# Optimization experiments

Hardware: AMD Instinct MI355X
Metric: run time of the kernel (lower is better)

## Reference

```python
import jax, jax.numpy as jnp
import numpy as np

B, D, H = 32768, 256, 256
LEAKY = 0.2  # tf.nn.leaky_relu default alpha


def setup_inputs() -> dict:
    key = jax.random.key(0)
    ks = jax.random.split(key, 12)
    s = 0.05  # weight scale (original inits comm net to zeros; random keeps grads nonzero)
    return {
        "x": jax.random.normal(ks[0], (B, D), jnp.float32),
        "visible_states_indices": jax.random.randint(ks[1], (B, 1), 0, B, jnp.int32),
        "real_step": jnp.ones((1,), jnp.bool_),
        "h": jax.random.normal(ks[2], (B, H), jnp.float32),
        "c": jax.random.normal(ks[3], (B, H), jnp.float32),
        "W1": s * jax.random.normal(ks[4], (2 * H, 512), jnp.float32),
        "b1": jnp.zeros((512,), jnp.float32),
        "W2": s * jax.random.normal(ks[5], (512, 512), jnp.float32),
        "b2": jnp.zeros((512,), jnp.float32),
        "W3": s * jax.random.normal(ks[6], (512, H), jnp.float32),
        "b3": jnp.zeros((H,), jnp.float32),
        "Wk": s * jax.random.normal(ks[7], (D, 4 * H), jnp.float32),
        "Wr": s * jax.random.normal(ks[8], (H, 4 * H), jnp.float32),
        "bl": jnp.zeros((4 * H,), jnp.float32),
    }


def reference(x, visible_states_indices, real_step, h, c,
              W1, b1, W2, b2, W3, b3, Wk, Wr, bl):
    vid = jnp.squeeze(visible_states_indices, axis=1)          # [B]
    rs = jnp.reshape(real_step, ())                            # scalar bool

    # gather neighbor comm states with a pad row for idx == -1
    padded = jnp.pad(h, ((1, 0), (0, 0)))                      # [B+1, H]
    gathered = jnp.take(padded, vid + 1, axis=0)               # [B, H]

    cs = jnp.concatenate([h, gathered], axis=-1)               # [B, 2H]
    for W, b in ((W1, b1), (W2, b2), (W3, b3)):
        cs = jax.nn.leaky_relu(cs @ W + b, negative_slope=LEAKY)

    # conditional scatter-combine back into the h state
    final_h = jnp.where((vid >= 0)[:, None], h + cs, h)        # [B, H]

    # wrapped LSTM cell (keras LSTMCell gate ordering i, f, g, o)
    z = x @ Wk + final_h @ Wr + bl                             # [B, 4H]
    i, f, g, o = jnp.split(z, 4, axis=-1)
    c_new = jax.nn.sigmoid(f) * c + jax.nn.sigmoid(i) * jnp.tanh(g)
    h_new = jax.nn.sigmoid(o) * jnp.tanh(c_new)
    outputs = h_new

    # only commit new states on real steps
    h_out = jnp.where(rs, h_new, final_h)
    c_out = jnp.where(rs, c_new, c)
    return outputs, h_out, c_out
```

## Files before the change

### kernel.cpp

```cpp
#include <hip/hip_runtime.h>
#include <stdint.h>

#define LEAKY 0.2f
#define NB 32768
#define HD 256

typedef __attribute__((ext_vector_type(8))) short short8;
typedef __attribute__((ext_vector_type(8))) unsigned short ushort8;
typedef __attribute__((ext_vector_type(4))) unsigned short ushort4v;
typedef __attribute__((ext_vector_type(4))) float f4;

static __device__ __forceinline__ float bf2f(unsigned short u) {
  union { unsigned int i; float f; } v; v.i = ((unsigned int)u) << 16; return v.f;
}
static __device__ __forceinline__ unsigned short f2bf(float f) {
  union { float f; unsigned int i; } v; v.f = f;
  return (unsigned short)((v.i + 0x7fffu + ((v.i >> 16) & 1u)) >> 16);
}
static __device__ __forceinline__ ushort8 pack8(f4 a, f4 b) {
  ushort8 o;
  o[0] = f2bf(a[0]); o[1] = f2bf(a[1]); o[2] = f2bf(a[2]); o[3] = f2bf(a[3]);
  o[4] = f2bf(b[0]); o[5] = f2bf(b[1]); o[6] = f2bf(b[2]); o[7] = f2bf(b[3]);
  return o;
}
static __device__ __forceinline__ float sigm(float x) { return 1.f / (1.f + __expf(-x)); }
static __device__ __forceinline__ float tanha(float x) {
  float e = __expf(2.f * x);
  return 1.f - 2.f / (e + 1.f);
}

__device__ __forceinline__ void gload16(const void* g, void* s) {
  __builtin_amdgcn_global_load_lds(
      (const __attribute__((address_space(1))) unsigned int*)g,
      (__attribute__((address_space(3))) unsigned int*)s, 16, 0, 0);
}


__global__ void wtrans(const float* __restrict__ W, unsigned short* __restrict__ Wt,
                       int K, int N) {
  int idx = blockIdx.x * 256 + threadIdx.x;
  if (idx >= K * N) return;
  int n = idx / K, k = idx - n * K;
  Wt[idx] = f2bf(W[(size_t)k * N + n]);
}

__global__ void wkrtrans(const float* __restrict__ Wk, const float* __restrict__ Wr,
                         unsigned short* __restrict__ Wt) {
  int idx = blockIdx.x * 256 + threadIdx.x;
  int n = idx >> 9, k = idx & 511;
  float v = (k < 256) ? Wk[(size_t)k * 1024 + n] : Wr[(size_t)(k - 256) * 1024 + n];
  Wt[idx] = f2bf(v);
}

__global__ void build_rows(const float* __restrict__ x, const float* __restrict__ h,
                           const int* __restrict__ vid,
                           unsigned short* __restrict__ catb,
                           unsigned short* __restrict__ csb) {
  int idx = blockIdx.x * 256 + threadIdx.x;
  int m = idx >> 5;
  int j = (idx & 31) << 3;
  f4 a0 = *(const f4*)(x + (size_t)m * 256 + j);
  f4 a1 = *(const f4*)(x + (size_t)m * 256 + j + 4);
  *(ushort8*)(catb + (size_t)m * 512 + j) = pack8(a0, a1);
  f4 h0 = *(const f4*)(h + (size_t)m * 256 + j);
  f4 h1 = *(const f4*)(h + (size_t)m * 256 + j + 4);
  *(ushort8*)(csb + (size_t)m * 512 + j) = pack8(h0, h1);
  int id = vid[m];
  f4 g0 = {0.f, 0.f, 0.f, 0.f}, g1 = {0.f, 0.f, 0.f, 0.f};
  if (id >= 0) {
    g0 = *(const f4*)(h + (size_t)id * 256 + j);
    g1 = *(const f4*)(h + (size_t)id * 256 + j + 4);
  }
  *(ushort8*)(csb + (size_t)m * 512 + 256 + j) = pack8(g0, g1);
}

template <int MODE>
__global__ __launch_bounds__(256, 2) void gemm_bf16(
    const unsigned short* __restrict__ A,
    const unsigned short* __restrict__ Bt,
    const float* __restrict__ bias,
    int nTn, int K,
    unsigned short* __restrict__ outb, int ldo, int col_off,
    float* __restrict__ outf,
    const float* __restrict__ hst,
    const int* __restrict__ vid) {
  __shared__ unsigned short sA[128 * 64];
  __shared__ unsigned short sB[128 * 64];

  const int t = threadIdx.x;
  const int tm = blockIdx.x / nTn;
  const int tn = blockIdx.x - tm * nTn;
  const int wid = t >> 6, lane = t & 63;
  const int wr = wid >> 1, wc = wid & 1;
  const int lrow = lane & 15, lkhi = lane >> 4;

  const unsigned short* Asrc = A + (size_t)tm * 128 * K;
  const unsigned short* Bsrc = Bt + (size_t)tn * 128 * K;
  const int rsub = t >> 3, slot = t & 7;

  f4 acc[4][4];
#pragma unroll
  for (int i = 0; i < 4; ++i)
#pragma unroll
    for (int j = 0; j < 4; ++j) acc[i][j] = {0.f, 0.f, 0.f, 0.f};

  for (int k0 = 0; k0 < K; k0 += 64) {
#pragma unroll
    for (int iss = 0; iss < 4; ++iss) {
      int r = iss * 32 + rsub;
      int gs = slot ^ (r & 7);
      gload16(Asrc + (size_t)r * K + k0 + gs * 8, (char*)sA + r * 128 + slot * 16);
      gload16(Bsrc + (size_t)r * K + k0 + gs * 8, (char*)sB + r * 128 + slot * 16);
    }
    __syncthreads();
#pragma unroll
    for (int kk = 0; kk < 2; ++kk) {
      short8 af[4], bf[4];
#pragma unroll
      for (int mi = 0; mi < 4; ++mi) {
        int row = wr * 64 + mi * 16 + lrow;
        int s = (kk * 4 + lkhi) ^ (row & 7);
        af[mi] = *(const short8*)&sA[row * 64 + s * 8];
      }
#pragma unroll
      for (int ni = 0; ni < 4; ++ni) {
        int rn = wc * 64 + ni * 16 + lrow;
        int s = (kk * 4 + lkhi) ^ (rn & 7);
        bf[ni] = *(const short8*)&sB[rn * 64 + s * 8];
      }
#pragma unroll
      for (int mi = 0; mi < 4; ++mi)
#pragma unroll
        for (int ni = 0; ni < 4; ++ni)
          acc[mi][ni] = __builtin_amdgcn_mfma_f32_16x16x32_bf16(af[mi], bf[ni],
                                                                acc[mi][ni], 0, 0, 0);
    }
    __syncthreads();
  }

  const int m_base = tm * 128 + wr * 64;
  const int n_base = tn * 128 + wc * 64;
  if (MODE == 1) {
#pragma unroll
    for (int mi = 0; mi < 4; ++mi) {
#pragma unroll
      for (int r = 0; r < 4; ++r) {
        int row = m_base + mi * 16 + lkhi * 4 + r;
        int id = vid[row];
#pragma unroll
        for (int ni = 0; ni < 4; ++ni) {
          int col = n_base + ni * 16 + lrow;
          float v = acc[mi][ni][r] + bias[col];
          v = v > 0.f ? v : LEAKY * v;
          float hv = hst[(size_t)row * HD + col];
          float fh = (id >= 0) ? hv + v : hv;
          outf[(size_t)row * HD + col] = fh;
          outb[(size_t)row * ldo + col_off + col] = f2bf(fh);
        }
      }
    }
  } else {
#pragma unroll
    for (int ni = 0; ni < 4; ++ni) {
      int col = n_base + ni * 16 + lrow;
      float bia = bias[col];
#pragma unroll
      for (int mi = 0; mi < 4; ++mi) {
#pragma unroll
        for (int r = 0; r < 4; ++r) {
          int row = m_base + mi * 16 + lkhi * 4 + r;
          float v = acc[mi][ni][r] + bia;
          if (MODE == 0) v = v > 0.f ? v : LEAKY * v;
          outb[(size_t)row * ldo + col_off + col] = f2bf(v);
        }
      }
    }
  }
}

__global__ void lstm_ew(const unsigned short* __restrict__ zb,
                        const float* __restrict__ cin,
                        const unsigned char* __restrict__ rs,
                        float* __restrict__ dout) {
  int idx = blockIdx.x * 256 + threadIdx.x;
  int m = idx >> 6;
  int n4 = (idx & 63) << 2;
  const unsigned short* zr = zb + (size_t)m * 1024 + n4;
  ushort4v zi = *(const ushort4v*)(zr);
  ushort4v zf = *(const ushort4v*)(zr + 256);
  ushort4v zg = *(const ushort4v*)(zr + 512);
  ushort4v zo = *(const ushort4v*)(zr + 768);
  size_t base = (size_t)m * HD + n4;
  float* outs = dout;
  float* houtp = dout + (size_t)NB * HD;
  float* coutp = dout + (size_t)2 * NB * HD;
  f4 c = *(const f4*)(cin + base);
  f4 fh = *(const f4*)(houtp + base);
  bool real = rs[0] != 0;
  f4 hn, ho, co;
#pragma unroll
  for (int e = 0; e < 4; ++e) {
    float i_ = sigm(bf2f(zi[e]));
    float f_ = sigm(bf2f(zf[e]));
    float g_ = tanha(bf2f(zg[e]));
    float o_ = sigm(bf2f(zo[e]));
    float cv = f_ * c[e] + i_ * g_;
    float hv = o_ * tanha(cv);
    hn[e] = hv;
    ho[e] = real ? hv : fh[e];
    co[e] = real ? cv : c[e];
  }
  *(f4*)(outs + base) = hn;
  *(f4*)(houtp + base) = ho;
  *(f4*)(coutp + base) = co;
}

extern "C" void kernel_launch(void* const* d_in, const int* in_sizes, int n_in,
                              void* d_out, int out_size, void* d_ws, size_t ws_size,
                              hipStream_t stream) {
  const float* x = (const float*)d_in[0];
  const int* vid = (const int*)d_in[1];
  const unsigned char* rs = (const unsigned char*)d_in[2];
  const float* h = (const float*)d_in[3];
  const float* c = (const float*)d_in[4];
  const float* W1 = (const float*)d_in[5];
  const float* b1 = (const float*)d_in[6];
  const float* W2 = (const float*)d_in[7];
  const float* b2 = (const float*)d_in[8];
  const float* W3 = (const float*)d_in[9];
  const float* b3 = (const float*)d_in[10];
  const float* Wk = (const float*)d_in[11];
  const float* Wr = (const float*)d_in[12];
  const float* bl = (const float*)d_in[13];
  float* dout = (float*)d_out;

  char* ws = (char*)d_ws;
  unsigned short* W1t = (unsigned short*)(ws);
  unsigned short* W2t = (unsigned short*)(ws + 524288);
  unsigned short* W3t = (unsigned short*)(ws + 1048576);
  unsigned short* Wkrt = (unsigned short*)(ws + 1310720);
  unsigned short* bufA = (unsigned short*)(ws + 2359296);
  unsigned short* bufB = (unsigned short*)(ws + 2359296 + 33554432);
  unsigned short* catb = (unsigned short*)(ws + 2359296 + 67108864);
  unsigned short* zb = bufA;

  float* fhout = dout + (size_t)NB * HD;

  wtrans<<<1024, 256, 0, stream>>>(W1, W1t, 512, 512);
  wtrans<<<1024, 256, 0, stream>>>(W2, W2t, 512, 512);
  wtrans<<<512, 256, 0, stream>>>(W3, W3t, 512, 256);
  wkrtrans<<<2048, 256, 0, stream>>>(Wk, Wr, Wkrt);
  build_rows<<<NB * 32 / 256, 256, 0, stream>>>(x, h, vid, catb, bufA);

  gemm_bf16<0><<<(NB / 128) * 4, 256, 0, stream>>>(bufA, W1t, b1, 4, 512,
                                                   bufB, 512, 0, nullptr, nullptr, nullptr);
  gemm_bf16<0><<<(NB / 128) * 4, 256, 0, stream>>>(bufB, W2t, b2, 4, 512,
                                                   bufA, 512, 0, nullptr, nullptr, nullptr);
  gemm_bf16<1><<<(NB / 128) * 2, 256, 0, stream>>>(bufA, W3t, b3, 2, 512,
                                                   catb, 512, 256, fhout, h, vid);
  gemm_bf16<2><<<(NB / 128) * 8, 256, 0, stream>>>(catb, Wkrt, bl, 8, 512,
                                                   zb, 1024, 0, nullptr, nullptr, nullptr);
  lstm_ew<<<NB * 64 / 256, 256, 0, stream>>>(zb, c, rs, dout);
}
```

Measured before the change: 367.6 us.

## Fuse LSTM gate math into final GEMM epilogue via permuted weight columns

Permutes the columns of the concatenated Wk/Wr weight so that each 128-column output tile holds the i, f, g and o gates for the same 32 hidden columns. The LSTM elementwise math can then run in the last GEMM's epilogue, and the separate lstm_ew kernel goes away. This removes the bf16 z buffer's write and re-read, one launch, and the rounding of z to bf16. The four weight-transpose kernels are also merged into one launch. The cost is a heavier epilogue with strided scalar stores and transcendental work in the GEMM kernel.

```diff
diff --git a/kernel.cpp b/kernel.cpp
--- a/kernel.cpp
+++ b/kernel.cpp
@@ -7,7 +7,6 @@
 
 typedef __attribute__((ext_vector_type(8))) short short8;
 typedef __attribute__((ext_vector_type(8))) unsigned short ushort8;
-typedef __attribute__((ext_vector_type(4))) unsigned short ushort4v;
 typedef __attribute__((ext_vector_type(4))) float f4;
 
 static __device__ __forceinline__ float bf2f(unsigned short u) {
@@ -35,21 +34,32 @@
       (__attribute__((address_space(3))) unsigned int*)s, 16, 0, 0);
 }
 
-
-__global__ void wtrans(const float* __restrict__ W, unsigned short* __restrict__ Wt,
-                       int K, int N) {
+__global__ void wprep(const float* __restrict__ W1, const float* __restrict__ W2,
+                      const float* __restrict__ W3, const float* __restrict__ Wk,
+                      const float* __restrict__ Wr,
+                      unsigned short* __restrict__ W1t, unsigned short* __restrict__ W2t,
+                      unsigned short* __restrict__ W3t, unsigned short* __restrict__ Wkrt) {
   int idx = blockIdx.x * 256 + threadIdx.x;
-  if (idx >= K * N) return;
-  int n = idx / K, k = idx - n * K;
-  Wt[idx] = f2bf(W[(size_t)k * N + n]);
-}
-
-__global__ void wkrtrans(const float* __restrict__ Wk, const float* __restrict__ Wr,
-                         unsigned short* __restrict__ Wt) {
-  int idx = blockIdx.x * 256 + threadIdx.x;
-  int n = idx >> 9, k = idx & 511;
-  float v = (k < 256) ? Wk[(size_t)k * 1024 + n] : Wr[(size_t)(k - 256) * 1024 + n];
-  Wt[idx] = f2bf(v);
+  if (idx < 262144) {
+    int n = idx >> 9, k = idx & 511;
+    W1t[idx] = f2bf(W1[k * 512 + n]);
+  } else if (idx < 524288) {
+    int j = idx - 262144;
+    int n = j >> 9, k = j & 511;
+    W2t[j] = f2bf(W2[k * 512 + n]);
+  } else if (idx < 655360) {
+    int j = idx - 524288;
+    int n = j >> 9, k = j & 511;
+    W3t[j] = f2bf(W3[k * 256 + n]);
+  } else {
+    int j = idx - 655360;
+    int rbt = j >> 9, k = j & 511;
+    int gate = (rbt >> 4) & 3;
+    int hcol = (rbt >> 7) * 32 + ((rbt >> 6) & 1) * 16 + (rbt & 15);
+    int ocol = gate * 256 + hcol;
+    float v = (k < 256) ? Wk[k * 1024 + ocol] : Wr[(k - 256) * 1024 + ocol];
+    Wkrt[j] = f2bf(v);
+  }
 }
 
 __global__ void build_rows(const float* __restrict__ x, const float* __restrict__ h,
@@ -83,7 +93,9 @@
     unsigned short* __restrict__ outb, int ldo, int col_off,
     float* __restrict__ outf,
     const float* __restrict__ hst,
-    const int* __restrict__ vid) {
+    const int* __restrict__ vid,
+    const float* __restrict__ cin,
+    const unsigned char* __restrict__ rsp) {
   __shared__ unsigned short sA[128 * 64];
   __shared__ unsigned short sB[128 * 64];
 
@@ -115,7 +127,7 @@
     __syncthreads();
 #pragma unroll
     for (int kk = 0; kk < 2; ++kk) {
-      short8 af[4], bf[4];
+      short8 af[4], bfr[4];
 #pragma unroll
       for (int mi = 0; mi < 4; ++mi) {
         int row = wr * 64 + mi * 16 + lrow;
@@ -126,13 +138,13 @@
       for (int ni = 0; ni < 4; ++ni) {
         int rn = wc * 64 + ni * 16 + lrow;
         int s = (kk * 4 + lkhi) ^ (rn & 7);
-        bf[ni] = *(const short8*)&sB[rn * 64 + s * 8];
+        bfr[ni] = *(const short8*)&sB[rn * 64 + s * 8];
       }
 #pragma unroll
       for (int mi = 0; mi < 4; ++mi)
 #pragma unroll
         for (int ni = 0; ni < 4; ++ni)
-          acc[mi][ni] = __builtin_amdgcn_mfma_f32_16x16x32_bf16(af[mi], bf[ni],
+          acc[mi][ni] = __builtin_amdgcn_mfma_f32_16x16x32_bf16(af[mi], bfr[ni],
                                                                 acc[mi][ni], 0, 0, 0);
     }
     __syncthreads();
@@ -159,6 +171,38 @@
         }
       }
     }
+  } else if (MODE == 3) {
+    const bool real = rsp[0] != 0;
+    const int hcol = tn * 32 + wc * 16 + lrow;
+    const float bi = bias[hcol];
+    const float bff = bias[256 + hcol];
+    const float bg = bias[512 + hcol];
+    const float bo = bias[768 + hcol];
+    float* outs = outf;
+    float* houtp = outf + (size_t)NB * HD;
+    float* coutp = outf + (size_t)2 * NB * HD;
+#pragma unroll
+    for (int mi = 0; mi < 4; ++mi) {
+#pragma unroll
+      for (int r = 0; r < 4; ++r) {
+        int row = m_base + mi * 16 + lkhi * 4 + r;
+        size_t base = (size_t)row * HD + hcol;
+        float cold = cin[base];
+        float i_ = sigm(acc[mi][0][r] + bi);
+        float f_ = sigm(acc[mi][1][r] + bff);
+        float g_ = tanha(acc[mi][2][r] + bg);
+        float o_ = sigm(acc[mi][3][r] + bo);
+        float cv = f_ * cold + i_ * g_;
+        float hv = o_ * tanha(cv);
+        outs[base] = hv;
+        if (real) {
+          houtp[base] = hv;
+          coutp[base] = cv;
+        } else {
+          coutp[base] = cold;
+        }
+      }
+    }
   } else {
 #pragma unroll
     for (int ni = 0; ni < 4; ++ni) {
@@ -170,49 +214,12 @@
         for (int r = 0; r < 4; ++r) {
           int row = m_base + mi * 16 + lkhi * 4 + r;
           float v = acc[mi][ni][r] + bia;
-          if (MODE == 0) v = v > 0.f ? v : LEAKY * v;
+          v = v > 0.f ? v : LEAKY * v;
           outb[(size_t)row * ldo + col_off + col] = f2bf(v);
         }
       }
     }
   }
-}
-
-__global__ void lstm_ew(const unsigned short* __restrict__ zb,
-                        const float* __restrict__ cin,
-                        const unsigned char* __restrict__ rs,
-                        float* __restrict__ dout) {
-  int idx = blockIdx.x * 256 + threadIdx.x;
-  int m = idx >> 6;
-  int n4 = (idx & 63) << 2;
-  const unsigned short* zr = zb + (size_t)m * 1024 + n4;
-  ushort4v zi = *(const ushort4v*)(zr);
-  ushort4v zf = *(const ushort4v*)(zr + 256);
-  ushort4v zg = *(const ushort4v*)(zr + 512);
-  ushort4v zo = *(const ushort4v*)(zr + 768);
-  size_t base = (size_t)m * HD + n4;
-  float* outs = dout;
-  float* houtp = dout + (size_t)NB * HD;
-  float* coutp = dout + (size_t)2 * NB * HD;
-  f4 c = *(const f4*)(cin + base);
-  f4 fh = *(const f4*)(houtp + base);
-  bool real = rs[0] != 0;
-  f4 hn, ho, co;
-#pragma unroll
-  for (int e = 0; e < 4; ++e) {
-    float i_ = sigm(bf2f(zi[e]));
-    float f_ = sigm(bf2f(zf[e]));
-    float g_ = tanha(bf2f(zg[e]));
-    float o_ = sigm(bf2f(zo[e]));
-    float cv = f_ * c[e] + i_ * g_;
-    float hv = o_ * tanha(cv);
-    hn[e] = hv;
-    ho[e] = real ? hv : fh[e];
-    co[e] = real ? cv : c[e];
-  }
-  *(f4*)(outs + base) = hn;
-  *(f4*)(houtp + base) = ho;
-  *(f4*)(coutp + base) = co;
 }
 
 extern "C" void kernel_launch(void* const* d_in, const int* in_sizes, int n_in,
@@ -242,23 +249,18 @@
   unsigned short* bufA = (unsigned short*)(ws + 2359296);
   unsigned short* bufB = (unsigned short*)(ws + 2359296 + 33554432);
   unsigned short* catb = (unsigned short*)(ws + 2359296 + 67108864);
-  unsigned short* zb = bufA;
 
   float* fhout = dout + (size_t)NB * HD;
 
-  wtrans<<<1024, 256, 0, stream>>>(W1, W1t, 512, 512);
-  wtrans<<<1024, 256, 0, stream>>>(W2, W2t, 512, 512);
-  wtrans<<<512, 256, 0, stream>>>(W3, W3t, 512, 256);
-  wkrtrans<<<2048, 256, 0, stream>>>(Wk, Wr, Wkrt);
+  wprep<<<4608, 256, 0, stream>>>(W1, W2, W3, Wk, Wr, W1t, W2t, W3t, Wkrt);
   build_rows<<<NB * 32 / 256, 256, 0, stream>>>(x, h, vid, catb, bufA);
 
-  gemm_bf16<0><<<(NB / 128) * 4, 256, 0, stream>>>(bufA, W1t, b1, 4, 512,
-                                                   bufB, 512, 0, nullptr, nullptr, nullptr);
-  gemm_bf16<0><<<(NB / 128) * 4, 256, 0, stream>>>(bufB, W2t, b2, 4, 512,
-                                                   bufA, 512, 0, nullptr, nullptr, nullptr);
-  gemm_bf16<1><<<(NB / 128) * 2, 256, 0, stream>>>(bufA, W3t, b3, 2, 512,
-                                                   catb, 512, 256, fhout, h, vid);
-  gemm_bf16<2><<<(NB / 128) * 8, 256, 0, stream>>>(catb, Wkrt, bl, 8, 512,
-                                                   zb, 1024, 0, nullptr, nullptr, nullptr);
-  lstm_ew<<<NB * 64 / 256, 256, 0, stream>>>(zb, c, rs, dout);
-}
+  gemm_bf16<0><<<(NB / 128) * 4, 256, 0, stream>>>(
+      bufA, W1t, b1, 4, 512, bufB, 512, 0, nullptr, nullptr, nullptr, nullptr, nullptr);
+  gemm_bf16<0><<<(NB / 128) * 4, 256, 0, stream>>>(
+      bufB, W2t, b2, 4, 512, bufA, 512, 0, nullptr, nullptr, nullptr, nullptr, nullptr);
+  gemm_bf16<1><<<(NB / 128) * 2, 256, 0, stream>>>(
+      bufA, W3t, b3, 2, 512, catb, 512, 256, fhout, h, vid, nullptr, nullptr);
+  gemm_bf16<3><<<(NB / 128) * 8, 256, 0, stream>>>(
+      catb, Wkrt, bl, 8, 512, nullptr, 0, 0, dout, nullptr, nullptr, c, rs);
+}
```

New measurement: 351.3 us. 1.05x faster.
